# Optimization experiments

Hardware: AMD Instinct MI355X
Metric: run time of the kernel (lower is better)

The kernel has to match this reference:

```python
import jax, jax.numpy as jnp
import numpy as np

N = 100000   # nodes
E = 1600000  # edges (avg degree 16)
D = 128      # input_dim == output_dim (residual requires equality)
BN_EPS = 1e-5


def setup_inputs() -> dict:
    key = jax.random.key(0)
    ks = jax.random.split(key, 8)
    X = jax.random.normal(ks[0], (N, D), dtype=jnp.float32)
    E_X = jax.random.normal(ks[1], (E, D), dtype=jnp.float32)
    snorm_n = jax.random.uniform(ks[2], (N, 1), dtype=jnp.float32)
    snorm_e = jax.random.uniform(ks[3], (E, 1), dtype=jnp.float32)
    src = jax.random.randint(ks[4], (E,), 0, N, dtype=jnp.int32)
    dst = jax.random.randint(ks[5], (E,), 0, N, dtype=jnp.int32)
    # Linear A and B parameters (torch nn.Linear: y = x @ W.T + b)
    scale = 1.0 / np.sqrt(D)
    A_w = jax.random.uniform(ks[6], (D, D), dtype=jnp.float32, minval=-scale, maxval=scale)
    B_w = jax.random.uniform(ks[7], (D, D), dtype=jnp.float32, minval=-scale, maxval=scale)
    A_b = jnp.zeros((D,), jnp.float32)
    B_b = jnp.zeros((D,), jnp.float32)
    # BatchNorm1d affine params (training mode -> batch stats)
    gamma = jnp.ones((D,), jnp.float32)
    beta = jnp.zeros((D,), jnp.float32)
    return {"X": X, "E_X": E_X, "snorm_n": snorm_n, "snorm_e": snorm_e,
            "src": src, "dst": dst, "A_w": A_w, "A_b": A_b,
            "B_w": B_w, "B_b": B_b, "gamma": gamma, "beta": beta}


def reference(X, E_X, snorm_n, snorm_e, src, dst, A_w, A_b, B_w, B_b, gamma, beta):
    AX = X @ A_w.T + A_b                       # [N, D]
    BX = X @ B_w.T + B_b                       # [N, D]
    # message: gather BX at edge sources; reduce: sum into destinations
    msgs = BX[src]                             # [E, D] irregular gather
    agg = jax.ops.segment_sum(msgs, dst, num_segments=N)  # [N, D]
    # DGL custom reduce only fires for nodes with in-degree > 0;
    # zero-in-degree nodes keep H = X
    indeg = jax.ops.segment_sum(jnp.ones((E,), X.dtype), dst, num_segments=N)
    H = jnp.where(indeg[:, None] > 0, AX + agg, X)
    H = H * snorm_n
    # BatchNorm1d (training mode: biased batch statistics)
    mean = jnp.mean(H, axis=0)
    var = jnp.mean((H - mean) ** 2, axis=0)
    H = (H - mean) * jax.lax.rsqrt(var + BN_EPS) * gamma + beta
    H = jax.nn.relu(H)
    H = X + H                                  # residual
    return (H, E_X)
```

## Files before the change

### kernel.cpp

```cpp
#include <hip/hip_runtime.h>

#define D 128
#define NNODES 100000
#define NEDGES 1600000
#define BN_EPS 1e-5f
#define NB_STATS 2048
#define NBLK_P 391

#define OFF_AX     0
#define OFF_BX16   12800000
#define OFF_ESRC   19200000
#define OFF_ORDER  20800000
#define OFF_INDEG  22400000
#define OFF_LEXC   22620000
#define OFF_BPART  22730000
#define OFF_BSCAN  22731000
#define OFF_PSUM   22740000
#define OFF_PSQ    23010000
#define OFF_SCALE  23280000
#define OFF_SHIFT  23280128
#define WS_NEED_BYTES 93200000ull

#define MAIN_GEMM 512
#define MAIN_EDGE 2048
#define MAIN_AGG  2048
#define MAIN_FIN  2048

static __device__ __forceinline__ unsigned short f2bf(float f) {
    unsigned int u = __float_as_uint(f);
    u = (u + 0x7FFF + ((u >> 16) & 1)) >> 16;
    return (unsigned short)u;
}
static __device__ __forceinline__ float bf_lo(unsigned v) {
    return __uint_as_float(v << 16);
}
static __device__ __forceinline__ float bf_hi(unsigned v) {
    return __uint_as_float(v & 0xFFFF0000u);
}

__global__ __launch_bounds__(256, 2) void gemm2_kernel(
    const float* __restrict__ X,
    const float* __restrict__ Aw, const float* __restrict__ Ab,
    const float* __restrict__ Bw, const float* __restrict__ Bb,
    float* __restrict__ AX, unsigned short* __restrict__ BX16)
{
    const bool isB = (blockIdx.x & 1);
    const float* __restrict__ W    = isB ? Bw : Aw;
    const float* __restrict__ bias = isB ? Bb : Ab;

    __shared__ float Ws[D * 132];
    const float4* W4 = (const float4*)W;
    for (int i = threadIdx.x; i < D * D / 4; i += 256) {
        int d  = i >> 5;
        int k4 = i & 31;
        float4 w = W4[i];
        *(float4*)&Ws[d * 132 + 4 * k4] = w;
    }
    __syncthreads();

    const int rg = threadIdx.x >> 5;
    const int cg = threadIdx.x & 31;

    float b[4];
#pragma unroll
    for (int j = 0; j < 4; ++j) b[j] = bias[cg + 32 * j];

    const int ntiles = NNODES / 32;
    for (int t = (blockIdx.x >> 1); t < ntiles; t += (MAIN_GEMM >> 1)) {
        const int row0 = t * 32 + rg * 4;
        float acc[4][4];
#pragma unroll
        for (int r = 0; r < 4; ++r)
#pragma unroll
            for (int j = 0; j < 4; ++j) acc[r][j] = b[j];

        const float* xbase = X + (size_t)row0 * D;
#pragma unroll 4
        for (int k = 0; k < D; k += 4) {
            float4 xr[4];
#pragma unroll
            for (int r = 0; r < 4; ++r)
                xr[r] = *(const float4*)&xbase[r * D + k];
            float4 wv[4];
#pragma unroll
            for (int j = 0; j < 4; ++j)
                wv[j] = *(const float4*)&Ws[(cg + 32 * j) * 132 + k];
#pragma unroll
            for (int r = 0; r < 4; ++r)
#pragma unroll
                for (int j = 0; j < 4; ++j)
                    acc[r][j] += xr[r].x * wv[j].x + xr[r].y * wv[j].y +
                                 xr[r].z * wv[j].z + xr[r].w * wv[j].w;
        }
        if (isB) {
#pragma unroll
            for (int r = 0; r < 4; ++r) {
                unsigned short* yrow = BX16 + (size_t)(row0 + r) * D;
#pragma unroll
                for (int j = 0; j < 4; ++j)
                    yrow[cg + 32 * j] = f2bf(acc[r][j]);
            }
        } else {
#pragma unroll
            for (int r = 0; r < 4; ++r) {
                float* yrow = AX + (size_t)(row0 + r) * D;
#pragma unroll
                for (int j = 0; j < 4; ++j) yrow[cg + 32 * j] = acc[r][j];
            }
        }
    }
}

__global__ __launch_bounds__(256) void hist_kernel(
    const int* __restrict__ dst, int* __restrict__ indeg,
    int* __restrict__ order)
{
    for (int e = blockIdx.x * 256 + threadIdx.x; e < NEDGES;
         e += MAIN_EDGE * 256)
        order[e] = atomicAdd(&indeg[dst[e]], 1);
}

__global__ __launch_bounds__(256) void scan1_kernel(
    const int* __restrict__ indeg, int* __restrict__ lexc,
    int* __restrict__ bpart)
{
    __shared__ int ls[256];
    const int i = blockIdx.x * 256 + threadIdx.x;
    const int v = (i < NNODES) ? indeg[i] : 0;
    ls[threadIdx.x] = v;
    __syncthreads();
    for (int off = 1; off < 256; off <<= 1) {
        int u = (threadIdx.x >= off) ? ls[threadIdx.x - off] : 0;
        __syncthreads();
        ls[threadIdx.x] += u;
        __syncthreads();
    }
    if (i < NNODES) lexc[i] = ls[threadIdx.x] - v;
    if (threadIdx.x == 255) bpart[blockIdx.x] = ls[255];
}

__global__ __launch_bounds__(512) void scan2_kernel(
    const int* __restrict__ bpart, int* __restrict__ bscan)
{
    __shared__ int ls[512];
    const int t = threadIdx.x;
    const int v = (t < NBLK_P) ? bpart[t] : 0;
    ls[t] = v;
    __syncthreads();
    for (int off = 1; off < 512; off <<= 1) {
        int u = (t >= off) ? ls[t - off] : 0;
        __syncthreads();
        ls[t] += u;
        __syncthreads();
    }
    if (t < NBLK_P) bscan[t] = ls[t] - v;
}

__global__ __launch_bounds__(256) void fill_kernel(
    const int* __restrict__ src, const int* __restrict__ dst,
    const int* __restrict__ bscan, const int* __restrict__ lexc,
    const int* __restrict__ order, int* __restrict__ esrc)
{
    for (int e = blockIdx.x * 256 + threadIdx.x; e < NEDGES;
         e += MAIN_EDGE * 256) {
        const int v = dst[e];
        esrc[bscan[v >> 8] + lexc[v] + order[e]] = src[e];
    }
}

__global__ __launch_bounds__(256, 8) void agg_kernel(
    const float4* __restrict__ AX4, const uint2* __restrict__ BX2,
    const float4* __restrict__ X4, const float* __restrict__ snorm,
    const int* __restrict__ bscan, const int* __restrict__ lexc,
    const int* __restrict__ indeg, const int* __restrict__ esrc,
    float4* __restrict__ Hpre4, float* __restrict__ psum,
    float* __restrict__ psq)
{
    const int w    = threadIdx.x >> 6;
    const int lane = threadIdx.x & 63;
    const int half = lane >> 5;
    const int hl   = lane & 31;
    float s0=0.f,s1=0.f,s2=0.f,s3=0.f, q0=0.f,q1=0.f,q2=0.f,q3=0.f;

    const int wid = blockIdx.x * 4 + w;
    for (int base = wid * 2; base < NNODES; base += MAIN_AGG * 8) {
        const int i = base + half;
        if (i < NNODES) {
            float a0, a1, a2, a3;
            const int deg = indeg[i];
            if (deg > 0) {
                const int rs = bscan[i >> 8] + lexc[i];
                float4 a = AX4[(size_t)i * 32 + hl];
                a0 = a.x; a1 = a.y; a2 = a.z; a3 = a.w;
                int e = rs;
                const int re = rs + deg;
                for (; e + 4 <= re; e += 4) {
                    const uint2 v0 = BX2[(size_t)esrc[e + 0] * 32 + hl];
                    const uint2 v1 = BX2[(size_t)esrc[e + 1] * 32 + hl];
                    const uint2 v2 = BX2[(size_t)esrc[e + 2] * 32 + hl];
                    const uint2 v3 = BX2[(size_t)esrc[e + 3] * 32 + hl];
                    a0 += bf_lo(v0.x)+bf_lo(v1.x)+bf_lo(v2.x)+bf_lo(v3.x);
                    a1 += bf_hi(v0.x)+bf_hi(v1.x)+bf_hi(v2.x)+bf_hi(v3.x);
                    a2 += bf_lo(v0.y)+bf_lo(v1.y)+bf_lo(v2.y)+bf_lo(v3.y);
                    a3 += bf_hi(v0.y)+bf_hi(v1.y)+bf_hi(v2.y)+bf_hi(v3.y);
                }
                for (; e < re; ++e) {
                    const uint2 v = BX2[(size_t)esrc[e] * 32 + hl];
                    a0 += bf_lo(v.x); a1 += bf_hi(v.x);
                    a2 += bf_lo(v.y); a3 += bf_hi(v.y);
                }
            } else {
                float4 x = X4[(size_t)i * 32 + hl];
                a0 = x.x; a1 = x.y; a2 = x.z; a3 = x.w;
            }
            const float sn = snorm[i];
            a0 *= sn; a1 *= sn; a2 *= sn; a3 *= sn;
            Hpre4[(size_t)i * 32 + hl] = make_float4(a0, a1, a2, a3);
            s0 += a0; s1 += a1; s2 += a2; s3 += a3;
            q0 += a0*a0; q1 += a1*a1; q2 += a2*a2; q3 += a3*a3;
        }
    }

    __shared__ float sp[4][64][4], sq[4][64][4];
    sp[w][lane][0]=s0; sp[w][lane][1]=s1; sp[w][lane][2]=s2; sp[w][lane][3]=s3;
    sq[w][lane][0]=q0; sq[w][lane][1]=q1; sq[w][lane][2]=q2; sq[w][lane][3]=q3;
    __syncthreads();
    if (threadIdx.x < D) {
        const int c  = threadIdx.x;
        const int l0 = c >> 2;
        const int j  = c & 3;
        float S = 0.f, Q = 0.f;
#pragma unroll
        for (int w2 = 0; w2 < 4; ++w2) {
            S += sp[w2][l0][j] + sp[w2][32 + l0][j];
            Q += sq[w2][l0][j] + sq[w2][32 + l0][j];
        }
        psum[blockIdx.x * D + c] = S;
        psq [blockIdx.x * D + c] = Q;
    }
}

__global__ __launch_bounds__(1024) void bnstats_kernel(
    const float* __restrict__ psum, const float* __restrict__ psq,
    const float* __restrict__ gamma, const float* __restrict__ beta,
    float* __restrict__ scale, float* __restrict__ shift)
{
    const int c = threadIdx.x & 127;
    const int g = threadIdx.x >> 7;
    float s = 0.f, q = 0.f;
    for (int b = g; b < NB_STATS; b += 8) {
        s += psum[b * D + c];
        q += psq [b * D + c];
    }
    __shared__ float ls[8][D], lq[8][D];
    ls[g][c] = s;
    lq[g][c] = q;
    __syncthreads();
    if (threadIdx.x < D) {
        float S = 0.f, Q = 0.f;
#pragma unroll
        for (int g2 = 0; g2 < 8; ++g2) { S += ls[g2][c]; Q += lq[g2][c]; }
        const float inv_n = 1.0f / (float)NNODES;
        float mean = S * inv_n;
        float var  = Q * inv_n - mean * mean;
        float sc   = rsqrtf(var + BN_EPS) * gamma[c];
        scale[c] = sc;
        shift[c] = beta[c] - mean * sc;
    }
}

__global__ __launch_bounds__(256) void final_kernel(
    const float* __restrict__ Hpre, const float* __restrict__ X,
    const float* __restrict__ scale, const float* __restrict__ shift,
    float* __restrict__ out)
{
    const int total = NNODES * D / 4;
    for (int i = blockIdx.x * 256 + threadIdx.x; i < total;
         i += MAIN_FIN * 256) {
        float4 h = ((const float4*)Hpre)[i];
        float4 x = ((const float4*)X)[i];
        int d0 = (i * 4) & 127;
        float4 r;
        r.x = x.x + fmaxf(0.f, h.x * scale[d0 + 0] + shift[d0 + 0]);
        r.y = x.y + fmaxf(0.f, h.y * scale[d0 + 1] + shift[d0 + 1]);
        r.z = x.z + fmaxf(0.f, h.z * scale[d0 + 2] + shift[d0 + 2]);
        r.w = x.w + fmaxf(0.f, h.w * scale[d0 + 3] + shift[d0 + 3]);
        ((float4*)out)[i] = r;
    }
}

extern "C" void kernel_launch(void* const* d_in, const int* in_sizes, int n_in,
                              void* d_out, int out_size, void* d_ws, size_t ws_size,
                              hipStream_t stream)
{
    const float* X       = (const float*)d_in[0];
    const float* E_X     = (const float*)d_in[1];
    const float* snorm_n = (const float*)d_in[2];
    const int*   src     = (const int*)d_in[4];
    const int*   dst     = (const int*)d_in[5];
    const float* A_w     = (const float*)d_in[6];
    const float* A_b     = (const float*)d_in[7];
    const float* B_w     = (const float*)d_in[8];
    const float* B_b     = (const float*)d_in[9];
    const float* gamma   = (const float*)d_in[10];
    const float* beta    = (const float*)d_in[11];

    float* out = (float*)d_out;
    const bool use_ws = (ws_size >= WS_NEED_BYTES);
    float* sb = use_ws ? (float*)d_ws : (out + (size_t)NNODES * D);

    float*          AX    = sb + OFF_AX;
    unsigned short* BX16  = (unsigned short*)(sb + OFF_BX16);
    int*            esrc  = (int*)(sb + OFF_ESRC);
    int*            order = (int*)(sb + OFF_ORDER);
    int*            indeg = (int*)(sb + OFF_INDEG);
    int*            lexc  = (int*)(sb + OFF_LEXC);
    int*            bpart = (int*)(sb + OFF_BPART);
    int*            bscan = (int*)(sb + OFF_BSCAN);
    float*          psum  = sb + OFF_PSUM;
    float*          psq   = sb + OFF_PSQ;
    float*          scale = sb + OFF_SCALE;
    float*          shift = sb + OFF_SHIFT;

    hipMemsetAsync(indeg, 0, NNODES * sizeof(int), stream);

    gemm2_kernel<<<MAIN_GEMM, 256, 0, stream>>>(
        X, A_w, A_b, B_w, B_b, AX, BX16);
    hist_kernel<<<MAIN_EDGE, 256, 0, stream>>>(dst, indeg, order);
    scan1_kernel<<<NBLK_P, 256, 0, stream>>>(indeg, lexc, bpart);
    scan2_kernel<<<1, 512, 0, stream>>>(bpart, bscan);
    fill_kernel<<<MAIN_EDGE, 256, 0, stream>>>(
        src, dst, bscan, lexc, order, esrc);
    agg_kernel<<<MAIN_AGG, 256, 0, stream>>>(
        (const float4*)AX, (const uint2*)BX16, (const float4*)X, snorm_n,
        bscan, lexc, indeg, esrc, (float4*)out, psum, psq);
    bnstats_kernel<<<1, 1024, 0, stream>>>(psum, psq, gamma, beta,
                                           scale, shift);
    final_kernel<<<MAIN_FIN, 256, 0, stream>>>(out, X, scale, shift, out);

    hipMemcpyAsync(out + (size_t)NNODES * D, E_X,
                   (size_t)NEDGES * D * sizeof(float),
                   hipMemcpyDeviceToDevice, stream);
}
```

Before: 752.7 us.

## Rewrite dual linear GEMM with bf16 MFMA and register-resident weights

The FP32 FMA GEMM that computed AX and BX is replaced by a bf16 MFMA (16x16x32) kernel. Each wave keeps its 64-column slice of A or B weights in registers as packed bf16 fragments, and one X tile is converted to bf16 in shared memory and shared by all four waves. X is now read once per tile for both outputs, where before it was read separately by the A and B blocks. The goal is to remove compute-bound scalar FMA work and halve X traffic, at the cost of bf16 rounding of X and W in the AX path, which was FP32 before.

```diff
diff --git a/kernel.cpp b/kernel.cpp
--- a/kernel.cpp
+++ b/kernel.cpp
@@ -6,6 +6,7 @@
 #define BN_EPS 1e-5f
 #define NB_STATS 2048
 #define NBLK_P 391
+#define NTILES 1563
 
 #define OFF_AX     0
 #define OFF_BX16   12800000
@@ -26,6 +27,9 @@
 #define MAIN_AGG  2048
 #define MAIN_FIN  2048
 
+typedef __attribute__((ext_vector_type(8))) short bf16x8;
+typedef __attribute__((ext_vector_type(4))) float f32x4;
+
 static __device__ __forceinline__ unsigned short f2bf(float f) {
     unsigned int u = __float_as_uint(f);
     u = (u + 0x7FFF + ((u >> 16) & 1)) >> 16;
@@ -36,6 +40,14 @@
 }
 static __device__ __forceinline__ float bf_hi(unsigned v) {
     return __uint_as_float(v & 0xFFFF0000u);
+}
+static __device__ __forceinline__ bf16x8 pack8(float4 a, float4 b) {
+    union { uint4 u; bf16x8 v; } r;
+    r.u.x = (unsigned)f2bf(a.x) | ((unsigned)f2bf(a.y) << 16);
+    r.u.y = (unsigned)f2bf(a.z) | ((unsigned)f2bf(a.w) << 16);
+    r.u.z = (unsigned)f2bf(b.x) | ((unsigned)f2bf(b.y) << 16);
+    r.u.w = (unsigned)f2bf(b.z) | ((unsigned)f2bf(b.w) << 16);
+    return r.v;
 }
 
 __global__ __launch_bounds__(256, 2) void gemm2_kernel(
@@ -44,68 +56,91 @@
     const float* __restrict__ Bw, const float* __restrict__ Bb,
     float* __restrict__ AX, unsigned short* __restrict__ BX16)
 {
-    const bool isB = (blockIdx.x & 1);
-    const float* __restrict__ W    = isB ? Bw : Aw;
+    __shared__ unsigned short Xs[64][136];
+
+    const int w    = threadIdx.x >> 6;
+    const int lane = threadIdx.x & 63;
+    const bool isB = (w >> 1);
+    const int colbase = (w & 1) * 64;
+    const int bn   = lane & 15;
+    const int kg   = lane >> 4;
+
+    const float* __restrict__ Wm   = isB ? Bw : Aw;
     const float* __restrict__ bias = isB ? Bb : Ab;
 
-    __shared__ float Ws[D * 132];
-    const float4* W4 = (const float4*)W;
-    for (int i = threadIdx.x; i < D * D / 4; i += 256) {
-        int d  = i >> 5;
-        int k4 = i & 31;
-        float4 w = W4[i];
-        *(float4*)&Ws[d * 132 + 4 * k4] = w;
-    }
-    __syncthreads();
-
-    const int rg = threadIdx.x >> 5;
-    const int cg = threadIdx.x & 31;
-
-    float b[4];
-#pragma unroll
-    for (int j = 0; j < 4; ++j) b[j] = bias[cg + 32 * j];
-
-    const int ntiles = NNODES / 32;
-    for (int t = (blockIdx.x >> 1); t < ntiles; t += (MAIN_GEMM >> 1)) {
-        const int row0 = t * 32 + rg * 4;
-        float acc[4][4];
-#pragma unroll
-        for (int r = 0; r < 4; ++r)
-#pragma unroll
-            for (int j = 0; j < 4; ++j) acc[r][j] = b[j];
-
-        const float* xbase = X + (size_t)row0 * D;
-#pragma unroll 4
-        for (int k = 0; k < D; k += 4) {
-            float4 xr[4];
-#pragma unroll
-            for (int r = 0; r < 4; ++r)
-                xr[r] = *(const float4*)&xbase[r * D + k];
-            float4 wv[4];
-#pragma unroll
-            for (int j = 0; j < 4; ++j)
-                wv[j] = *(const float4*)&Ws[(cg + 32 * j) * 132 + k];
-#pragma unroll
-            for (int r = 0; r < 4; ++r)
-#pragma unroll
-                for (int j = 0; j < 4; ++j)
-                    acc[r][j] += xr[r].x * wv[j].x + xr[r].y * wv[j].y +
-                                 xr[r].z * wv[j].z + xr[r].w * wv[j].w;
-        }
-        if (isB) {
+    bf16x8 wf[4][4];
+#pragma unroll
+    for (int ks = 0; ks < 4; ++ks)
+#pragma unroll
+        for (int ct = 0; ct < 4; ++ct) {
+            const int d = colbase + ct * 16 + bn;
+            const int k = ks * 32 + kg * 8;
+            const float4* wp = (const float4*)&Wm[d * D + k];
+            wf[ks][ct] = pack8(wp[0], wp[1]);
+        }
+
+    float bias4[4];
+#pragma unroll
+    for (int ct = 0; ct < 4; ++ct) bias4[ct] = bias[colbase + ct * 16 + bn];
+
+    for (int t = blockIdx.x; t < NTILES; t += MAIN_GEMM) {
+        const int row0 = t * 64;
+        for (int c = threadIdx.x; c < 1024; c += 256) {
+            const int r   = c >> 4;
+            const int col = (c & 15) * 8;
+            const int row = min(row0 + r, NNODES - 1);
+            const float4* xp = (const float4*)&X[(size_t)row * D + col];
+            const float4 x0 = xp[0], x1 = xp[1];
+            union { uint4 u; } pk;
+            pk.u.x = (unsigned)f2bf(x0.x) | ((unsigned)f2bf(x0.y) << 16);
+            pk.u.y = (unsigned)f2bf(x0.z) | ((unsigned)f2bf(x0.w) << 16);
+            pk.u.z = (unsigned)f2bf(x1.x) | ((unsigned)f2bf(x1.y) << 16);
+            pk.u.w = (unsigned)f2bf(x1.z) | ((unsigned)f2bf(x1.w) << 16);
+            *(uint4*)&Xs[r][col] = pk.u;
+        }
+        __syncthreads();
+
+        f32x4 acc[4][4];
+#pragma unroll
+        for (int rt = 0; rt < 4; ++rt)
+#pragma unroll
+            for (int ct = 0; ct < 4; ++ct)
+                acc[rt][ct] = (f32x4){0.f, 0.f, 0.f, 0.f};
+
+#pragma unroll
+        for (int ks = 0; ks < 4; ++ks) {
+            bf16x8 a[4];
+#pragma unroll
+            for (int rt = 0; rt < 4; ++rt)
+                a[rt] = *(const bf16x8*)&Xs[rt * 16 + bn][ks * 32 + kg * 8];
+#pragma unroll
+            for (int rt = 0; rt < 4; ++rt)
+#pragma unroll
+                for (int ct = 0; ct < 4; ++ct)
+                    acc[rt][ct] = __builtin_amdgcn_mfma_f32_16x16x32_bf16(
+                        a[rt], wf[ks][ct], acc[rt][ct], 0, 0, 0);
+        }
+        __syncthreads();
+
+#pragma unroll
+        for (int rt = 0; rt < 4; ++rt) {
 #pragma unroll
             for (int r = 0; r < 4; ++r) {
-                unsigned short* yrow = BX16 + (size_t)(row0 + r) * D;
-#pragma unroll
-                for (int j = 0; j < 4; ++j)
-                    yrow[cg + 32 * j] = f2bf(acc[r][j]);
-            }
-        } else {
-#pragma unroll
-            for (int r = 0; r < 4; ++r) {
-                float* yrow = AX + (size_t)(row0 + r) * D;
-#pragma unroll
-                for (int j = 0; j < 4; ++j) yrow[cg + 32 * j] = acc[r][j];
+                const int row = row0 + rt * 16 + kg * 4 + r;
+                if (row < NNODES) {
+                    if (!isB) {
+                        float* yrow = AX + (size_t)row * D + colbase;
+#pragma unroll
+                        for (int ct = 0; ct < 4; ++ct)
+                            yrow[ct * 16 + bn] = acc[rt][ct][r] + bias4[ct];
+                    } else {
+                        unsigned short* yrow = BX16 + (size_t)row * D + colbase;
+#pragma unroll
+                        for (int ct = 0; ct < 4; ++ct)
+                            yrow[ct * 16 + bn] =
+                                f2bf(acc[rt][ct][r] + bias4[ct]);
+                    }
+                }
             }
         }
     }
```

Result: faster. 659.4 us (-12.4%).
